# Optimization experiments

Hardware: AMD Instinct MI355X
Metric: run time of the kernel (lower is better)

Reference implementation:

```python
import jax, jax.numpy as jnp
import numpy as np

M, N, E, IN, C, HID, TOPK = 4, 50000, 400000, 128, 128, 256, 2
NEG_SLOPE = 0.2


def setup_inputs() -> dict:
    key = jax.random.key(0)
    k = jax.random.split(key, 16)
    s = lambda f: 1.0 / np.sqrt(f)
    return {
        "x_src": jax.random.normal(k[0], (M, N, IN), jnp.float32),
        "x_dst": jax.random.normal(k[1], (N, IN), jnp.float32),
        "src_idx": jax.random.randint(k[2], (M, E), 0, N),
        "dst_idx": jax.random.randint(k[3], (M, E), 0, N),
        "proj_Ws": jax.random.normal(k[4], (M, IN, C), jnp.float32) * s(IN),
        "proj_bs": jnp.zeros((M, C), jnp.float32),
        "projd_W": jax.random.normal(k[5], (IN, C), jnp.float32) * s(IN),
        "projd_b": jnp.zeros((C,), jnp.float32),
        "lin_src": jax.random.normal(k[6], (M, C), jnp.float32) * s(C),
        "lin_dst": jax.random.normal(k[7], (M, C), jnp.float32) * s(C),
        "gm_W1": jax.random.normal(k[8], (C, C), jnp.float32) * s(C),
        "gm_b1": jnp.zeros((C,), jnp.float32),
        "gm_W2": jax.random.normal(k[9], (C, C), jnp.float32) * s(C),
        "gm_b2": jnp.zeros((C,), jnp.float32),
        "gate_W1": jax.random.normal(k[10], (M * C, HID), jnp.float32) * s(M * C),
        "gate_b1": jnp.zeros((HID,), jnp.float32),
        "gate_W2": jax.random.normal(k[11], (HID, M), jnp.float32) * s(HID),
        "gate_b2": jnp.zeros((M,), jnp.float32),
        "exp_W1": jax.random.normal(k[12], (M, C, HID), jnp.float32) * s(C),
        "exp_b1": jnp.zeros((M, HID), jnp.float32),
        "exp_W2": jax.random.normal(k[13], (M, HID, C), jnp.float32) * s(HID),
        "exp_b2": jnp.zeros((M, C), jnp.float32),
    }


def _propagate(xs_t, asrc_t, adst_t, si, di, recept_t):
    # GAT-style attention message passing for one edge type.
    # xs_t: [N,C] projected src feats, asrc_t/adst_t: [N] attn logits,
    # si/di: [E] edge endpoints, recept_t: [N] per-dst-node receptivity gate.
    e = jax.nn.leaky_relu(asrc_t[si] + adst_t[di], NEG_SLOPE)  # [E]
    emax = jax.ops.segment_max(e, di, num_segments=N)
    ez = jnp.exp(e - emax[di])
    den = jax.ops.segment_sum(ez, di, num_segments=N)
    alpha = ez / (den[di] + 1e-16)                             # softmax per dst node
    msg = xs_t[si] * (alpha * recept_t[di])[:, None]           # [E,C]
    return jax.ops.segment_sum(msg, di, num_segments=N)       # [N,C]


def reference(x_src, x_dst, src_idx, dst_idx, proj_Ws, proj_bs, projd_W, projd_b,
              lin_src, lin_dst, gm_W1, gm_b1, gm_W2, gm_b2,
              gate_W1, gate_b1, gate_W2, gate_b2,
              exp_W1, exp_b1, exp_W2, exp_b2):
    # --- SynapticConvLayer (eval path, heads=1) ---
    xs = jnp.einsum('mni,mic->mnc', x_src, proj_Ws) + proj_bs[:, None, :]  # [M,N,C]
    xd = x_dst @ projd_W + projd_b                                          # [N,C]
    a_src = jnp.einsum('mnc,mc->mn', xs, lin_src)
    a_dst = jnp.einsum('nc,mc->mn', xd[None].repeat(M, 0) * 0 + xd[None], lin_dst) if False else jnp.einsum('nc,mc->mn', xd, lin_dst)
    prop = jax.vmap(_propagate)
    out1 = prop(xs, a_src, a_dst, src_idx, dst_idx, jnp.ones((M, N), xs.dtype))
    # receptivity from grad_map surrogate (inference branch)
    feat_diff = out1 - xd[None]                                            # [M,N,C]
    mo = jax.nn.sigmoid(jax.nn.relu(feat_diff @ gm_W1 + gm_b1) @ gm_W2 + gm_b2)
    gd = (mo * feat_diff).mean(axis=-1)                                    # [M,N]
    recept = gd / (jnp.abs(gd) + 1e-8)                                     # L2-norm over the singleton head dim == abs
    out2 = prop(xs, a_src, a_dst, src_idx, dst_idx, recept)
    feats = jax.nn.relu(out2)                                              # [M,N,C] per-edge-type dst features
    # --- SourceExpertMoE ---
    feats_nm = feats.transpose(1, 0, 2)                                    # [N,M,C]
    gate_in = feats_nm.reshape(N, M * C)
    logits = jax.nn.relu(gate_in @ gate_W1 + gate_b1) @ gate_W2 + gate_b2
    gw = jax.nn.softmax(logits, axis=1)
    scores = gw + recept.T                                                 # gate weights + receptivity
    top_w, top_i = jax.lax.top_k(scores, TOPK)
    top_w = top_w / top_w.sum(axis=1, keepdims=True)
    # expert e applied to source-e features for every node (dense, then gather top-k)
    h = jax.nn.relu(jnp.einsum('nmi,mih->nmh', feats_nm, exp_W1) + exp_b1)
    out_all = jnp.einsum('nmh,mho->nmo', h, exp_W2) + exp_b2               # [N,M,C]
    sel = jnp.take_along_axis(out_all, top_i[:, :, None], axis=1)          # [N,K,C]
    final = (sel * top_w[:, :, None]).sum(axis=1)                          # [N,C]
    return final
```

## Files before the change

### kernel.cpp

```cpp
#include <hip/hip_runtime.h>
#include <hip/hip_bf16.h>
#include <math.h>

#define M_  4
#define N_  50000
#define E_  400000
#define IN_ 128
#define C_  128
#define HID_ 256

template<int AMODE, int EPI, int ASCALE>
__global__ void __launch_bounds__(256) gemm8(
    const float* A, const float* A2, const float* __restrict__ B,
    const float* __restrict__ bias, float* Cmat,
    const float* __restrict__ rowscale, const int* __restrict__ idx,
    const int* __restrict__ cnts, const float* __restrict__ AS,
    const float* __restrict__ fdbuf, const int* __restrict__ roff,
    int R, int K, int NC,
    long long aBatch, long long bBatch, int biasBatch, long long cBatch,
    long long strideM)
{
  __shared__ float As[8][128];
  __shared__ float Bs[8][128];
  __shared__ float red[(EPI == 5) ? 128 * 17 : 1];

  const int tid = threadIdx.x;
  const int b = blockIdx.y;
  const int Reff = (AMODE == 4 || AMODE == 5) ? cnts[b] : (cnts ? cnts[0] : R);
  const int rb = blockIdx.x * 128;
  if (rb >= Reff) return;
  const int cb = blockIdx.z * 128;

  const float* Ab = (AMODE == 2) ? A : (A + (long long)b * aBatch);
  const float* Bb = B + (long long)b * bBatch + cb;
  const float* biasb = bias + (long long)b * biasBatch + cb;

  const int ar = tid >> 1;
  const int ak = (tid & 1) * 4;
  const int r_a = rb + ar;
  const bool a_ok = (r_a < Reff);
  long long a_row = 0;
  float a_rs = 0.f;
  if (a_ok) {
    if (AMODE == 3) {
      int orow = idx[r_a];
      a_row = (long long)orow * K;
      if (ASCALE == 2) a_rs = AS[orow];
    } else if (AMODE == 4) {
      int orow = idx[(long long)b * N_ + r_a];
      a_row = (long long)orow * K;
      if (ASCALE == 2) a_rs = AS[(long long)b * N_ + orow];
    } else if (AMODE == 5) {
      a_row = (long long)(roff[b] + r_a) * K;
    } else if (AMODE == 2) {
      a_row = (long long)r_a * 128;
    } else {
      a_row = (long long)r_a * K;
    }
  }
  const int bk = tid >> 5;
  const int bc = (tid & 31) * 4;

  const int tx = tid & 15;
  const int ty = tid >> 4;

  float acc[8][8];
  #pragma unroll
  for (int i = 0; i < 8; ++i)
    #pragma unroll
    for (int j = 0; j < 8; ++j) acc[i][j] = 0.f;

  const int nt = K >> 3;
  float4 av = make_float4(0.f, 0.f, 0.f, 0.f), bv;

  if (a_ok) {
    if (AMODE == 2) {
      av = *(const float4*)(Ab + (long long)(ak >> 7) * strideM + a_row + (ak & 127));
      if (ASCALE == 1) {
        float rs = AS[(ak >> 7) * N_ + r_a];
        av.x = fmaxf(av.x * rs, 0.f); av.y = fmaxf(av.y * rs, 0.f);
        av.z = fmaxf(av.z * rs, 0.f); av.w = fmaxf(av.w * rs, 0.f);
      }
    } else {
      av = *(const float4*)(Ab + a_row + ak);
      if (AMODE == 1) {
        float4 y = *(const float4*)(A2 + (long long)r_a * 128 + ak);
        av.x -= y.x; av.y -= y.y; av.z -= y.z; av.w -= y.w;
      }
      if ((AMODE == 3 || AMODE == 4) && ASCALE == 2) {
        av.x = fmaxf(av.x * a_rs, 0.f); av.y = fmaxf(av.y * a_rs, 0.f);
        av.z = fmaxf(av.z * a_rs, 0.f); av.w = fmaxf(av.w * a_rs, 0.f);
      }
    }
  }
  bv = *(const float4*)(Bb + (long long)bk * NC + bc);

  for (int t = 0; t < nt; ++t) {
    __syncthreads();
    As[ak + 0][ar] = av.x; As[ak + 1][ar] = av.y;
    As[ak + 2][ar] = av.z; As[ak + 3][ar] = av.w;
    *(float4*)(&Bs[bk][bc]) = bv;
    __syncthreads();

    if (t + 1 < nt) {
      const int k0 = (t + 1) * 8;
      if (a_ok) {
        if (AMODE == 2) {
          int kk0 = k0 + ak;
          av = *(const float4*)(Ab + (long long)(kk0 >> 7) * strideM + a_row + (kk0 & 127));
          if (ASCALE == 1) {
            float rs = AS[(kk0 >> 7) * N_ + r_a];
            av.x = fmaxf(av.x * rs, 0.f); av.y = fmaxf(av.y * rs, 0.f);
            av.z = fmaxf(av.z * rs, 0.f); av.w = fmaxf(av.w * rs, 0.f);
          }
        } else {
          av = *(const float4*)(Ab + a_row + k0 + ak);
          if (AMODE == 1) {
            float4 y = *(const float4*)(A2 + (long long)r_a * 128 + k0 + ak);
            av.x -= y.x; av.y -= y.y; av.z -= y.z; av.w -= y.w;
          }
          if ((AMODE == 3 || AMODE == 4) && ASCALE == 2) {
            av.x = fmaxf(av.x * a_rs, 0.f); av.y = fmaxf(av.y * a_rs, 0.f);
            av.z = fmaxf(av.z * a_rs, 0.f); av.w = fmaxf(av.w * a_rs, 0.f);
          }
        }
      }
      bv = *(const float4*)(Bb + (long long)(k0 + bk) * NC + bc);
    }

    #pragma unroll
    for (int kk = 0; kk < 8; ++kk) {
      float4 alo = *(float4*)(&As[kk][ty * 4]);
      float4 ahi = *(float4*)(&As[kk][64 + ty * 4]);
      float4 blo = *(float4*)(&Bs[kk][tx * 4]);
      float4 bhi = *(float4*)(&Bs[kk][64 + tx * 4]);
      float a8[8] = {alo.x, alo.y, alo.z, alo.w, ahi.x, ahi.y, ahi.z, ahi.w};
      float b8[8] = {blo.x, blo.y, blo.z, blo.w, bhi.x, bhi.y, bhi.z, bhi.w};
      #pragma unroll
      for (int i = 0; i < 8; ++i)
        #pragma unroll
        for (int j = 0; j < 8; ++j)
          acc[i][j] += a8[i] * b8[j];
    }
  }

  if (EPI == 5) {
    #pragma unroll
    for (int i = 0; i < 8; ++i) {
      const int r_local = (i < 4 ? ty * 4 + i : 64 + ty * 4 + (i - 4));
      const int r = rb + r_local;
      if (r < Reff) {
        const float* fdrow = fdbuf + (long long)b * cBatch + (long long)r * 128;
        const float* xdrow = A2 + (long long)r * 128;
        float4 flo = *(const float4*)(fdrow + tx * 4);
        float4 fhi = *(const float4*)(fdrow + 64 + tx * 4);
        float4 xlo = *(const float4*)(xdrow + tx * 4);
        float4 xhi = *(const float4*)(xdrow + 64 + tx * 4);
        float fd8[8] = {flo.x - xlo.x, flo.y - xlo.y, flo.z - xlo.z, flo.w - xlo.w,
                        fhi.x - xhi.x, fhi.y - xhi.y, fhi.z - xhi.z, fhi.w - xhi.w};
        float p = 0.f;
        #pragma unroll
        for (int j = 0; j < 8; ++j) {
          const int c = (j < 4 ? tx * 4 + j : 64 + tx * 4 + (j - 4));
          float mo = 1.f / (1.f + expf(-(acc[i][j] + biasb[c])));
          p += mo * fd8[j];
        }
        red[r_local * 17 + tx] = p;
      }
    }
    __syncthreads();
    if (tid < 128) {
      const int r = rb + tid;
      if (r < Reff) {
        float s = 0.f;
        #pragma unroll
        for (int t = 0; t < 16; ++t) s += red[tid * 17 + t];
        float gd = s / 128.f;
        Cmat[(long long)b * N_ + r] = gd / (fabsf(gd) + 1e-8f);
      }
    }
    return;
  }

  #pragma unroll
  for (int i = 0; i < 8; ++i) {
    const int r = rb + (i < 4 ? ty * 4 + i : 64 + ty * 4 + (i - 4));
    if (r >= Reff) continue;
    long long crow;
    float w = 0.f;
    if (EPI == 4) {
      int orow = idx[r];
      w = rowscale[orow];
      crow = (long long)orow * NC + cb;
    } else if (EPI == 8) {
      int orow = idx[(long long)b * N_ + r];
      w = rowscale[(long long)b * N_ + orow];
      crow = (long long)orow * 128 + cb;
    } else if (EPI == 7) {
      crow = (long long)(roff[b] + r) * NC + cb;
    } else {
      crow = (long long)b * cBatch + (long long)r * NC + cb;
    }
    #pragma unroll
    for (int j = 0; j < 8; ++j) {
      const int c = (j < 4 ? tx * 4 + j : 64 + tx * 4 + (j - 4));
      float v = acc[i][j] + biasb[c];
      if (EPI == 1 || EPI == 7) v = fmaxf(v, 0.f);
      if (EPI == 2) v = 1.f / (1.f + expf(-v));
      if (EPI == 4) Cmat[crow + c] += w * v;
      else if (EPI == 8) atomicAdd(&Cmat[crow + c], w * v);
      else Cmat[crow + c] = v;
    }
  }
}

__global__ void attn_logit_kernel(const float* __restrict__ X, const float* __restrict__ lin,
                                  float* __restrict__ out, int Nn, int perM)
{
  int m = blockIdx.y;
  int w = blockIdx.x * (blockDim.x >> 6) + (threadIdx.x >> 6);
  int lane = threadIdx.x & 63;
  if (w >= Nn) return;
  long long row = perM ? ((long long)m * Nn + w) : (long long)w;
  const float* xr = X + row * 128;
  const float* lr = lin + m * 128;
  float acc = xr[lane] * lr[lane] + xr[lane + 64] * lr[lane + 64];
  #pragma unroll
  for (int off = 32; off > 0; off >>= 1) acc += __shfl_down(acc, off);
  if (lane == 0) out[(long long)m * Nn + w] = acc;
}

__global__ void count_kernel(const int* __restrict__ dst, int* __restrict__ cnt, int Nn)
{
  int e = blockIdx.x * blockDim.x + threadIdx.x;
  int m = blockIdx.y;
  if (e >= E_) return;
  atomicAdd(&cnt[(long long)m * Nn + dst[(long long)m * E_ + e]], 1);
}

__global__ void chunkscan_kernel(const int* __restrict__ cnt, int* __restrict__ rowptr,
                                 int* __restrict__ chunktot)
{
  int m = blockIdx.y, ch = blockIdx.x;
  int base = ch * 1024;
  const int* c = cnt + (long long)m * N_;
  int* rp = rowptr + (long long)m * (N_ + 1);
  __shared__ int sums[256];
  int t = threadIdx.x;
  int v[4]; int s = 0;
  #pragma unroll
  for (int k = 0; k < 4; ++k) {
    int i = base + t * 4 + k;
    v[k] = (i < N_) ? c[i] : 0;
    s += v[k];
  }
  sums[t] = s;
  __syncthreads();
  for (int off = 1; off < 256; off <<= 1) {
    int x = (t >= off) ? sums[t - off] : 0;
    __syncthreads();
    sums[t] += x;
    __syncthreads();
  }
  int run = sums[t] - s;
  #pragma unroll
  for (int k = 0; k < 4; ++k) {
    int i = base + t * 4 + k;
    run += v[k];
    if (i < N_) rp[i + 1] = run;
  }
  if (t == 255) chunktot[m * 64 + ch] = sums[255];
}

__global__ void scantot_kernel(int* __restrict__ chunktot, int nch)
{
  int m = threadIdx.x;
  if (m >= M_) return;
  int run = 0;
  for (int ch = 0; ch < nch; ++ch) {
    int v = chunktot[m * 64 + ch];
    chunktot[m * 64 + ch] = run;
    run += v;
  }
}

__global__ void addoff_kernel(int* __restrict__ rowptr, const int* __restrict__ chunktot)
{
  int m = blockIdx.y, ch = blockIdx.x;
  int off = chunktot[m * 64 + ch];
  int t = threadIdx.x;
  int* rp = rowptr + (long long)m * (N_ + 1);
  #pragma unroll
  for (int k = 0; k < 4; ++k) {
    int i = ch * 1024 + t * 4 + k;
    if (i < N_) rp[i + 1] += off;
  }
  if (ch == 0 && t == 0) rp[0] = 0;
}

__global__ void scatter_kernel(const int* __restrict__ dst, const int* __restrict__ rowptr,
                               int* __restrict__ fill, int* __restrict__ col, int Nn)
{
  int e = blockIdx.x * blockDim.x + threadIdx.x;
  int m = blockIdx.y;
  if (e >= E_) return;
  int d = dst[(long long)m * E_ + e];
  int pos = rowptr[(long long)m * (Nn + 1) + d] + atomicAdd(&fill[(long long)m * Nn + d], 1);
  col[(long long)m * E_ + pos] = e;
}

__global__ void sortbucket_kernel(const int* __restrict__ rowptr, int* __restrict__ col, int Nn)
{
  int n = blockIdx.x * blockDim.x + threadIdx.x;
  int m = blockIdx.y;
  if (n >= Nn) return;
  const int* rp = rowptr + (long long)m * (Nn + 1);
  int* c = col + (long long)m * E_;
  int b = rp[n], e = rp[n + 1];
  for (int i = b + 1; i < e; ++i) {
    int v = c[i]; int j = i - 1;
    while (j >= b && c[j] > v) { c[j + 1] = c[j]; --j; }
    c[j + 1] = v;
  }
}

__global__ void edge_e_kernel(const int* __restrict__ src, const int* __restrict__ dst,
                              const float* __restrict__ asrc, const float* __restrict__ adst,
                              float* __restrict__ e_edge)
{
  int e = blockIdx.x * blockDim.x + threadIdx.x;
  int m = blockIdx.y;
  if (e >= E_) return;
  long long off = (long long)m * E_ + e;
  float v = asrc[(long long)m * N_ + src[off]] + adst[(long long)m * N_ + dst[off]];
  e_edge[off] = (v >= 0.f) ? v : 0.2f * v;
}

__global__ void alpha_kernel(const int* __restrict__ rowptr, const int* __restrict__ col,
                             const int* __restrict__ src, const float* __restrict__ e_edge,
                             float* __restrict__ alpha, int* __restrict__ src_csr)
{
  int n = blockIdx.x * blockDim.x + threadIdx.x;
  int m = blockIdx.y;
  if (n >= N_) return;
  const int* rp = rowptr + (long long)m * (N_ + 1);
  const int* cl = col + (long long)m * E_;
  const int* sr = src + (long long)m * E_;
  const float* ee = e_edge + (long long)m * E_;
  float* al = alpha + (long long)m * E_;
  int* sc = src_csr + (long long)m * E_;
  int b = rp[n], en = rp[n + 1];
  if (b == en) return;
  float emax = -INFINITY;
  for (int j = b; j < en; ++j) emax = fmaxf(emax, ee[cl[j]]);
  float den = 0.f;
  for (int j = b; j < en; ++j) {
    int eid = cl[j];
    float ez = expf(ee[eid] - emax);
    den += ez;
    al[j] = ez;
    sc[j] = sr[eid];
  }
  float inv = 1.f / (den + 1e-16f);
  for (int j = b; j < en; ++j) al[j] *= inv;
}

__global__ void prop2_kernel(const float* __restrict__ xs, const int* __restrict__ rowptr,
                             const float* __restrict__ alpha, const int* __restrict__ src_csr,
                             float* __restrict__ out)
{
  int d = blockIdx.x * 2 + (threadIdx.x >> 7);
  int m = blockIdx.y;
  int c = threadIdx.x & 127;
  if (d >= N_) return;
  const int* rp = rowptr + (long long)m * (N_ + 1);
  const float* al = alpha + (long long)m * E_;
  const int* sc = src_csr + (long long)m * E_;
  const float* xsm = xs + (long long)m * N_ * 128;
  int b = rp[d], en = rp[d + 1];
  float acc = 0.f;
  int j = b;
  for (; j + 3 < en; j += 4) {
    float a0 = al[j], a1 = al[j + 1], a2 = al[j + 2], a3 = al[j + 3];
    int s0 = sc[j], s1 = sc[j + 1], s2 = sc[j + 2], s3 = sc[j + 3];
    float x0 = xsm[(long long)s0 * 128 + c];
    float x1 = xsm[(long long)s1 * 128 + c];
    float x2 = xsm[(long long)s2 * 128 + c];
    float x3 = xsm[(long long)s3 * 128 + c];
    acc += a0 * x0; acc += a1 * x1; acc += a2 * x2; acc += a3 * x3;
  }
  for (; j < en; ++j)
    acc += al[j] * xsm[(long long)sc[j] * 128 + c];
  out[((long long)m * N_ + d) * 128 + c] = acc;
}

__global__ void gate_logits_kernel(const float* __restrict__ h, const float* __restrict__ W2,
                                   const float* __restrict__ b2, float* __restrict__ logits, int Nn)
{
  int w = blockIdx.x * (blockDim.x >> 6) + (threadIdx.x >> 6);
  int lane = threadIdx.x & 63;
  if (w >= Nn) return;
  const float* hr = h + (long long)w * 256;
  float a0 = 0.f, a1 = 0.f, a2 = 0.f, a3 = 0.f;
  for (int j = lane; j < 256; j += 64) {
    float hv = hr[j];
    a0 += hv * W2[j * 4 + 0];
    a1 += hv * W2[j * 4 + 1];
    a2 += hv * W2[j * 4 + 2];
    a3 += hv * W2[j * 4 + 3];
  }
  #pragma unroll
  for (int off = 32; off > 0; off >>= 1) {
    a0 += __shfl_down(a0, off);
    a1 += __shfl_down(a1, off);
    a2 += __shfl_down(a2, off);
    a3 += __shfl_down(a3, off);
  }
  if (lane == 0) {
    long long o = (long long)w * 4;
    logits[o + 0] = a0 + b2[0];
    logits[o + 1] = a1 + b2[1];
    logits[o + 2] = a2 + b2[2];
    logits[o + 3] = a3 + b2[3];
  }
}

__global__ void topk_kernel(const float* __restrict__ logits, const float* __restrict__ recept,
                            float* __restrict__ wsel, int Nn)
{
  int n = blockIdx.x * blockDim.x + threadIdx.x;
  if (n >= Nn) return;
  float l[4];
  #pragma unroll
  for (int m = 0; m < 4; ++m) l[m] = logits[(long long)n * 4 + m];
  float mx = fmaxf(fmaxf(l[0], l[1]), fmaxf(l[2], l[3]));
  float e[4], s = 0.f;
  #pragma unroll
  for (int m = 0; m < 4; ++m) { e[m] = expf(l[m] - mx); s += e[m]; }
  float sc[4];
  #pragma unroll
  for (int m = 0; m < 4; ++m) sc[m] = e[m] / s + recept[(long long)m * Nn + n];
  int i0 = 0; float v0 = sc[0];
  #pragma unroll
  for (int m = 1; m < 4; ++m) if (sc[m] > v0) { v0 = sc[m]; i0 = m; }
  int i1 = -1; float v1 = -INFINITY;
  #pragma unroll
  for (int m = 0; m < 4; ++m) { if (m == i0) continue; if (sc[m] > v1) { v1 = sc[m]; i1 = m; } }
  float ts = v0 + v1;
  float w0 = v0 / ts, w1 = v1 / ts;
  #pragma unroll
  for (int m = 0; m < 4; ++m)
    wsel[(long long)m * Nn + n] = (m == i0) ? w0 : ((m == i1) ? w1 : 0.f);
}

__global__ void compact_kernel(const float* __restrict__ wsel, int* __restrict__ idx,
                               int* __restrict__ cnts, int Nn)
{
  int n = blockIdx.x * blockDim.x + threadIdx.x;
  if (n >= Nn) return;
  #pragma unroll
  for (int m = 0; m < 4; ++m) {
    if (wsel[(long long)m * Nn + n] != 0.f) {
      int p = atomicAdd(&cnts[m], 1);
      idx[(long long)m * Nn + p] = n;
    }
  }
}

__global__ void prefix4_kernel(const int* __restrict__ cnts, int* __restrict__ off)
{
  if (threadIdx.x == 0) {
    int r = 0;
    #pragma unroll
    for (int m = 0; m < 4; ++m) { off[m] = r; r += cnts[m]; }
  }
}

extern "C" void kernel_launch(void* const* d_in, const int* in_sizes, int n_in,
                              void* d_out, int out_size, void* d_ws, size_t ws_size,
                              hipStream_t stream) {
  const float* x_src   = (const float*)d_in[0];
  const float* x_dst   = (const float*)d_in[1];
  const int*   src_idx = (const int*)d_in[2];
  const int*   dst_idx = (const int*)d_in[3];
  const float* proj_Ws = (const float*)d_in[4];
  const float* proj_bs = (const float*)d_in[5];
  const float* projd_W = (const float*)d_in[6];
  const float* projd_b = (const float*)d_in[7];
  const float* lin_src = (const float*)d_in[8];
  const float* lin_dst = (const float*)d_in[9];
  const float* gm_W1   = (const float*)d_in[10];
  const float* gm_b1   = (const float*)d_in[11];
  const float* gm_W2   = (const float*)d_in[12];
  const float* gm_b2   = (const float*)d_in[13];
  const float* gate_W1 = (const float*)d_in[14];
  const float* gate_b1 = (const float*)d_in[15];
  const float* gate_W2 = (const float*)d_in[16];
  const float* gate_b2 = (const float*)d_in[17];
  const float* exp_W1  = (const float*)d_in[18];
  const float* exp_b1  = (const float*)d_in[19];
  const float* exp_W2  = (const float*)d_in[20];
  const float* exp_b2  = (const float*)d_in[21];
  float* final_out = (float*)d_out;

  float* ws = (float*)d_ws;
  float* bufA   = ws;
  float* bufB   = ws + 25600000LL;
  float* xd     = ws + 51200000LL;
  float* asrc   = ws + 57600000LL;
  float* adst   = ws + 57800000LL;
  float* recept = ws + 58000000LL;
  float* wsel   = ws + 58200000LL;
  float* logits = ws + 58400000LL;
  float* e_edge = ws + 58600000LL;
  float* alpha  = ws + 60200000LL;
  int*   ibase  = (int*)(ws + 61800000LL);
  int*   rowptr = ibase;
  int*   col    = ibase + 200004;
  int*   cnt    = ibase + 1800004;
  int*   expidx = cnt;
  int*   expcnt = ibase + 2000004;
  int*   src_csr= ibase + 2000008;
  int*   chunktot = ibase + 3600008;
  int*   expoff = ibase + 3600264;

  const long long NC = (long long)N_ * C_;
  const int RB = (N_ + 127) / 128;
  const int NCH = (N_ + 1023) / 1024;

  hipMemsetAsync(d_out, 0, (size_t)out_size * sizeof(float), stream);

  hipMemsetAsync(cnt, 0, (size_t)M_ * N_ * sizeof(int), stream);
  count_kernel<<<dim3((E_ + 255) / 256, M_), 256, 0, stream>>>(dst_idx, cnt, N_);
  chunkscan_kernel<<<dim3(NCH, M_), 256, 0, stream>>>(cnt, rowptr, chunktot);
  scantot_kernel<<<1, 64, 0, stream>>>(chunktot, NCH);
  addoff_kernel<<<dim3(NCH, M_), 256, 0, stream>>>(rowptr, chunktot);
  hipMemsetAsync(cnt, 0, (size_t)M_ * N_ * sizeof(int), stream);
  scatter_kernel<<<dim3((E_ + 255) / 256, M_), 256, 0, stream>>>(dst_idx, rowptr, cnt, col, N_);
  sortbucket_kernel<<<dim3((N_ + 255) / 256, M_), 256, 0, stream>>>(rowptr, col, N_);

  gemm8<0, 0, 0><<<dim3(RB, 1, 1), 256, 0, stream>>>(
      x_dst, nullptr, projd_W, projd_b, xd, nullptr, nullptr, nullptr, nullptr, nullptr,
      nullptr, N_, IN_, C_, 0, 0, 0, 0, 0);
  attn_logit_kernel<<<dim3((N_ + 3) / 4, M_), 256, 0, stream>>>(xd, lin_dst, adst, N_, 0);

  gemm8<0, 0, 0><<<dim3(RB, M_, 1), 256, 0, stream>>>(
      x_src, nullptr, proj_Ws, proj_bs, bufA, nullptr, nullptr, nullptr, nullptr, nullptr,
      nullptr, N_, IN_, C_, NC, (long long)IN_ * C_, C_, NC, 0);
  attn_logit_kernel<<<dim3((N_ + 3) / 4, M_), 256, 0, stream>>>(bufA, lin_src, asrc, N_, 1);

  edge_e_kernel<<<dim3((E_ + 255) / 256, M_), 256, 0, stream>>>(
      src_idx, dst_idx, asrc, adst, e_edge);
  alpha_kernel<<<dim3((N_ + 255) / 256, M_), 256, 0, stream>>>(
      rowptr, col, src_idx, e_edge, alpha, src_csr);

  prop2_kernel<<<dim3((N_ + 1) / 2, M_), 256, 0, stream>>>(bufA, rowptr, alpha, src_csr, bufB);

  gemm8<1, 1, 0><<<dim3(RB, M_, 1), 256, 0, stream>>>(
      bufB, xd, gm_W1, gm_b1, bufA, nullptr, nullptr, nullptr, nullptr, nullptr,
      nullptr, N_, C_, C_, NC, 0, 0, NC, 0);
  gemm8<0, 5, 0><<<dim3(RB, M_, 1), 256, 0, stream>>>(
      bufA, xd, gm_W2, gm_b2, recept, nullptr, nullptr, nullptr, nullptr, bufB,
      nullptr, N_, C_, C_, NC, 0, 0, NC, 0);

  gemm8<2, 1, 1><<<dim3(RB, 1, 2), 256, 0, stream>>>(
      bufB, nullptr, gate_W1, gate_b1, bufA, nullptr, nullptr, nullptr, recept, nullptr,
      nullptr, N_, M_ * C_, HID_, 0, 0, 0, 0, NC);
  gate_logits_kernel<<<dim3((N_ + 3) / 4), 256, 0, stream>>>(bufA, gate_W2, gate_b2, logits, N_);
  topk_kernel<<<(N_ + 255) / 256, 256, 0, stream>>>(logits, recept, wsel, N_);

  hipMemsetAsync(expcnt, 0, 4 * sizeof(int), stream);
  compact_kernel<<<(N_ + 255) / 256, 256, 0, stream>>>(wsel, expidx, expcnt, N_);
  prefix4_kernel<<<1, 64, 0, stream>>>(expcnt, expoff);

  gemm8<4, 7, 2><<<dim3(RB, M_, 2), 256, 0, stream>>>(
      bufB, nullptr, exp_W1, exp_b1, bufA, nullptr,
      expidx, expcnt, recept, nullptr, expoff,
      N_, C_, HID_, NC, (long long)C_ * HID_, HID_, 0, 0);
  gemm8<5, 8, 0><<<dim3(RB, M_, 1), 256, 0, stream>>>(
      bufA, nullptr, exp_W2, exp_b2, final_out, wsel,
      expidx, expcnt, nullptr, nullptr, expoff,
      N_, HID_, C_, 0, (long long)HID_ * C_, C_, 0, 0);
}
```

Before: 1.379 ms.

## Double-buffer GEMM shared tiles and replace atomic expert scatter with combine kernel

The GEMM now ping-pongs two shared-memory tile buffers, so each k-step needs one barrier instead of two and the next tile's global loads overlap the current FMAs. The expert second-layer GEMM writes dense per-expert outputs into a compact buffer instead of atomically adding weighted rows into the output. A new combine kernel then gathers each node's selected expert rows via a recorded position map and sums them with the gate weights. This drops the output memset and the atomics, but adds an extra kernel pass and doubles the shared memory for the tiles.

```diff
diff --git a/kernel.cpp b/kernel.cpp
--- a/kernel.cpp
+++ b/kernel.cpp
@@ -10,18 +10,18 @@
 #define HID_ 256
 
 template<int AMODE, int EPI, int ASCALE>
-__global__ void __launch_bounds__(256) gemm8(
+__global__ void __launch_bounds__(256) gemm9(
     const float* A, const float* A2, const float* __restrict__ B,
     const float* __restrict__ bias, float* Cmat,
-    const float* __restrict__ rowscale, const int* __restrict__ idx,
-    const int* __restrict__ cnts, const float* __restrict__ AS,
-    const float* __restrict__ fdbuf, const int* __restrict__ roff,
+    const int* __restrict__ idx, const int* __restrict__ cnts,
+    const float* __restrict__ AS, const float* __restrict__ fdbuf,
+    const int* __restrict__ roff,
     int R, int K, int NC,
     long long aBatch, long long bBatch, int biasBatch, long long cBatch,
     long long strideM)
 {
-  __shared__ float As[8][128];
-  __shared__ float Bs[8][128];
+  __shared__ float As[2][8][128];
+  __shared__ float Bs[2][8][128];
   __shared__ float red[(EPI == 5) ? 128 * 17 : 1];
 
   const int tid = threadIdx.x;
@@ -42,11 +42,7 @@
   long long a_row = 0;
   float a_rs = 0.f;
   if (a_ok) {
-    if (AMODE == 3) {
-      int orow = idx[r_a];
-      a_row = (long long)orow * K;
-      if (ASCALE == 2) a_rs = AS[orow];
-    } else if (AMODE == 4) {
+    if (AMODE == 4) {
       int orow = idx[(long long)b * N_ + r_a];
       a_row = (long long)orow * K;
       if (ASCALE == 2) a_rs = AS[(long long)b * N_ + orow];
@@ -73,67 +69,57 @@
   const int nt = K >> 3;
   float4 av = make_float4(0.f, 0.f, 0.f, 0.f), bv;
 
-  if (a_ok) {
-    if (AMODE == 2) {
-      av = *(const float4*)(Ab + (long long)(ak >> 7) * strideM + a_row + (ak & 127));
-      if (ASCALE == 1) {
-        float rs = AS[(ak >> 7) * N_ + r_a];
-        av.x = fmaxf(av.x * rs, 0.f); av.y = fmaxf(av.y * rs, 0.f);
-        av.z = fmaxf(av.z * rs, 0.f); av.w = fmaxf(av.w * rs, 0.f);
-      }
-    } else {
-      av = *(const float4*)(Ab + a_row + ak);
-      if (AMODE == 1) {
-        float4 y = *(const float4*)(A2 + (long long)r_a * 128 + ak);
-        av.x -= y.x; av.y -= y.y; av.z -= y.z; av.w -= y.w;
-      }
-      if ((AMODE == 3 || AMODE == 4) && ASCALE == 2) {
-        av.x = fmaxf(av.x * a_rs, 0.f); av.y = fmaxf(av.y * a_rs, 0.f);
-        av.z = fmaxf(av.z * a_rs, 0.f); av.w = fmaxf(av.w * a_rs, 0.f);
-      }
-    }
-  }
-  bv = *(const float4*)(Bb + (long long)bk * NC + bc);
+#define LOAD_TILE(k0)                                                          \
+  {                                                                            \
+    if (a_ok) {                                                                \
+      if (AMODE == 2) {                                                        \
+        int kk0 = (k0) + ak;                                                   \
+        av = *(const float4*)(Ab + (long long)(kk0 >> 7) * strideM + a_row +   \
+                              (kk0 & 127));                                    \
+        if (ASCALE == 1) {                                                     \
+          float rs = AS[(kk0 >> 7) * N_ + r_a];                                \
+          av.x = fmaxf(av.x * rs, 0.f); av.y = fmaxf(av.y * rs, 0.f);          \
+          av.z = fmaxf(av.z * rs, 0.f); av.w = fmaxf(av.w * rs, 0.f);          \
+        }                                                                      \
+      } else {                                                                 \
+        av = *(const float4*)(Ab + a_row + (k0) + ak);                         \
+        if (AMODE == 1) {                                                      \
+          float4 y = *(const float4*)(A2 + (long long)r_a * 128 + (k0) + ak);  \
+          av.x -= y.x; av.y -= y.y; av.z -= y.z; av.w -= y.w;                  \
+        }                                                                      \
+        if (AMODE == 4 && ASCALE == 2) {                                       \
+          av.x = fmaxf(av.x * a_rs, 0.f); av.y = fmaxf(av.y * a_rs, 0.f);      \
+          av.z = fmaxf(av.z * a_rs, 0.f); av.w = fmaxf(av.w * a_rs, 0.f);      \
+        }                                                                      \
+      }                                                                        \
+    } else {                                                                   \
+      av = make_float4(0.f, 0.f, 0.f, 0.f);                                    \
+    }                                                                          \
+    bv = *(const float4*)(Bb + (long long)((k0) + bk) * NC + bc);              \
+  }
+
+#define WRITE_TILE(buf)                                                        \
+  {                                                                            \
+    As[buf][ak + 0][ar] = av.x; As[buf][ak + 1][ar] = av.y;                    \
+    As[buf][ak + 2][ar] = av.z; As[buf][ak + 3][ar] = av.w;                    \
+    *(float4*)(&Bs[buf][bk][bc]) = bv;                                         \
+  }
+
+  LOAD_TILE(0)
+  WRITE_TILE(0)
 
   for (int t = 0; t < nt; ++t) {
     __syncthreads();
-    As[ak + 0][ar] = av.x; As[ak + 1][ar] = av.y;
-    As[ak + 2][ar] = av.z; As[ak + 3][ar] = av.w;
-    *(float4*)(&Bs[bk][bc]) = bv;
-    __syncthreads();
-
-    if (t + 1 < nt) {
-      const int k0 = (t + 1) * 8;
-      if (a_ok) {
-        if (AMODE == 2) {
-          int kk0 = k0 + ak;
-          av = *(const float4*)(Ab + (long long)(kk0 >> 7) * strideM + a_row + (kk0 & 127));
-          if (ASCALE == 1) {
-            float rs = AS[(kk0 >> 7) * N_ + r_a];
-            av.x = fmaxf(av.x * rs, 0.f); av.y = fmaxf(av.y * rs, 0.f);
-            av.z = fmaxf(av.z * rs, 0.f); av.w = fmaxf(av.w * rs, 0.f);
-          }
-        } else {
-          av = *(const float4*)(Ab + a_row + k0 + ak);
-          if (AMODE == 1) {
-            float4 y = *(const float4*)(A2 + (long long)r_a * 128 + k0 + ak);
-            av.x -= y.x; av.y -= y.y; av.z -= y.z; av.w -= y.w;
-          }
-          if ((AMODE == 3 || AMODE == 4) && ASCALE == 2) {
-            av.x = fmaxf(av.x * a_rs, 0.f); av.y = fmaxf(av.y * a_rs, 0.f);
-            av.z = fmaxf(av.z * a_rs, 0.f); av.w = fmaxf(av.w * a_rs, 0.f);
-          }
-        }
-      }
-      bv = *(const float4*)(Bb + (long long)(k0 + bk) * NC + bc);
-    }
+    const int cur = t & 1;
+    const bool more = (t + 1 < nt);
+    if (more) LOAD_TILE((t + 1) * 8)
 
     #pragma unroll
     for (int kk = 0; kk < 8; ++kk) {
-      float4 alo = *(float4*)(&As[kk][ty * 4]);
-      float4 ahi = *(float4*)(&As[kk][64 + ty * 4]);
-      float4 blo = *(float4*)(&Bs[kk][tx * 4]);
-      float4 bhi = *(float4*)(&Bs[kk][64 + tx * 4]);
+      float4 alo = *(float4*)(&As[cur][kk][ty * 4]);
+      float4 ahi = *(float4*)(&As[cur][kk][64 + ty * 4]);
+      float4 blo = *(float4*)(&Bs[cur][kk][tx * 4]);
+      float4 bhi = *(float4*)(&Bs[cur][kk][64 + tx * 4]);
       float a8[8] = {alo.x, alo.y, alo.z, alo.w, ahi.x, ahi.y, ahi.z, ahi.w};
       float b8[8] = {blo.x, blo.y, blo.z, blo.w, bhi.x, bhi.y, bhi.z, bhi.w};
       #pragma unroll
@@ -142,7 +128,11 @@
         for (int j = 0; j < 8; ++j)
           acc[i][j] += a8[i] * b8[j];
     }
-  }
+
+    if (more) WRITE_TILE(cur ^ 1)
+  }
+#undef LOAD_TILE
+#undef WRITE_TILE
 
   if (EPI == 5) {
     #pragma unroll
@@ -187,29 +177,15 @@
     const int r = rb + (i < 4 ? ty * 4 + i : 64 + ty * 4 + (i - 4));
     if (r >= Reff) continue;
     long long crow;
-    float w = 0.f;
-    if (EPI == 4) {
-      int orow = idx[r];
-      w = rowscale[orow];
-      crow = (long long)orow * NC + cb;
-    } else if (EPI == 8) {
-      int orow = idx[(long long)b * N_ + r];
-      w = rowscale[(long long)b * N_ + orow];
-      crow = (long long)orow * 128 + cb;
-    } else if (EPI == 7) {
-      crow = (long long)(roff[b] + r) * NC + cb;
-    } else {
-      crow = (long long)b * cBatch + (long long)r * NC + cb;
-    }
+    if (EPI == 7) crow = (long long)(roff[b] + r) * NC + cb;
+    else if (EPI == 9) crow = (long long)(roff[b] + r) * 128 + cb;
+    else crow = (long long)b * cBatch + (long long)r * NC + cb;
     #pragma unroll
     for (int j = 0; j < 8; ++j) {
       const int c = (j < 4 ? tx * 4 + j : 64 + tx * 4 + (j - 4));
       float v = acc[i][j] + biasb[c];
       if (EPI == 1 || EPI == 7) v = fmaxf(v, 0.f);
-      if (EPI == 2) v = 1.f / (1.f + expf(-v));
-      if (EPI == 4) Cmat[crow + c] += w * v;
-      else if (EPI == 8) atomicAdd(&Cmat[crow + c], w * v);
-      else Cmat[crow + c] = v;
+      Cmat[crow + c] = v;
     }
   }
 }
@@ -454,7 +430,7 @@
 }
 
 __global__ void compact_kernel(const float* __restrict__ wsel, int* __restrict__ idx,
-                               int* __restrict__ cnts, int Nn)
+                               int* __restrict__ posmn, int* __restrict__ cnts, int Nn)
 {
   int n = blockIdx.x * blockDim.x + threadIdx.x;
   if (n >= Nn) return;
@@ -463,6 +439,7 @@
     if (wsel[(long long)m * Nn + n] != 0.f) {
       int p = atomicAdd(&cnts[m], 1);
       idx[(long long)m * Nn + p] = n;
+      posmn[(long long)m * Nn + n] = p;
     }
   }
 }
@@ -474,6 +451,27 @@
     #pragma unroll
     for (int m = 0; m < 4; ++m) { off[m] = r; r += cnts[m]; }
   }
+}
+
+__global__ void combine_kernel(const float* __restrict__ outp, const float* __restrict__ wsel,
+                               const int* __restrict__ posmn, const int* __restrict__ expoff,
+                               float* __restrict__ fin)
+{
+  long long i = (long long)blockIdx.x * blockDim.x + threadIdx.x;
+  if (i >= (long long)N_ * 32) return;
+  int n = (int)(i >> 5);
+  int c4 = (int)(i & 31) * 4;
+  float4 acc = make_float4(0.f, 0.f, 0.f, 0.f);
+  #pragma unroll
+  for (int m = 0; m < 4; ++m) {
+    float w = wsel[(long long)m * N_ + n];
+    if (w != 0.f) {
+      int p = expoff[m] + posmn[(long long)m * N_ + n];
+      float4 v = *(const float4*)(outp + (long long)p * 128 + c4);
+      acc.x += w * v.x; acc.y += w * v.y; acc.z += w * v.z; acc.w += w * v.w;
+    }
+  }
+  *(float4*)(fin + (long long)n * 128 + c4) = acc;
 }
 
 extern "C" void kernel_launch(void* const* d_in, const int* in_sizes, int n_in,
@@ -523,12 +521,11 @@
   int*   src_csr= ibase + 2000008;
   int*   chunktot = ibase + 3600008;
   int*   expoff = ibase + 3600264;
+  int*   posmn  = ibase + 3600268;
 
   const long long NC = (long long)N_ * C_;
   const int RB = (N_ + 127) / 128;
   const int NCH = (N_ + 1023) / 1024;
-
-  hipMemsetAsync(d_out, 0, (size_t)out_size * sizeof(float), stream);
 
   hipMemsetAsync(cnt, 0, (size_t)M_ * N_ * sizeof(int), stream);
   count_kernel<<<dim3((E_ + 255) / 256, M_), 256, 0, stream>>>(dst_idx, cnt, N_);
@@ -539,13 +536,13 @@
   scatter_kernel<<<dim3((E_ + 255) / 256, M_), 256, 0, stream>>>(dst_idx, rowptr, cnt, col, N_);
   sortbucket_kernel<<<dim3((N_ + 255) / 256, M_), 256, 0, stream>>>(rowptr, col, N_);
 
-  gemm8<0, 0, 0><<<dim3(RB, 1, 1), 256, 0, stream>>>(
-      x_dst, nullptr, projd_W, projd_b, xd, nullptr, nullptr, nullptr, nullptr, nullptr,
+  gemm9<0, 0, 0><<<dim3(RB, 1, 1), 256, 0, stream>>>(
+      x_dst, nullptr, projd_W, projd_b, xd, nullptr, nullptr, nullptr, nullptr,
       nullptr, N_, IN_, C_, 0, 0, 0, 0, 0);
   attn_logit_kernel<<<dim3((N_ + 3) / 4, M_), 256, 0, stream>>>(xd, lin_dst, adst, N_, 0);
 
-  gemm8<0, 0, 0><<<dim3(RB, M_, 1), 256, 0, stream>>>(
-      x_src, nullptr, proj_Ws, proj_bs, bufA, nullptr, nullptr, nullptr, nullptr, nullptr,
+  gemm9<0, 0, 0><<<dim3(RB, M_, 1), 256, 0, stream>>>(
+      x_src, nullptr, proj_Ws, proj_bs, bufA, nullptr, nullptr, nullptr, nullptr,
       nullptr, N_, IN_, C_, NC, (long long)IN_ * C_, C_, NC, 0);
   attn_logit_kernel<<<dim3((N_ + 3) / 4, M_), 256, 0, stream>>>(bufA, lin_src, asrc, N_, 1);
 
@@ -556,29 +553,29 @@
 
   prop2_kernel<<<dim3((N_ + 1) / 2, M_), 256, 0, stream>>>(bufA, rowptr, alpha, src_csr, bufB);
 
-  gemm8<1, 1, 0><<<dim3(RB, M_, 1), 256, 0, stream>>>(
-      bufB, xd, gm_W1, gm_b1, bufA, nullptr, nullptr, nullptr, nullptr, nullptr,
+  gemm9<1, 1, 0><<<dim3(RB, M_, 1), 256, 0, stream>>>(
+      bufB, xd, gm_W1, gm_b1, bufA, nullptr, nullptr, nullptr, nullptr,
       nullptr, N_, C_, C_, NC, 0, 0, NC, 0);
-  gemm8<0, 5, 0><<<dim3(RB, M_, 1), 256, 0, stream>>>(
-      bufA, xd, gm_W2, gm_b2, recept, nullptr, nullptr, nullptr, nullptr, bufB,
+  gemm9<0, 5, 0><<<dim3(RB, M_, 1), 256, 0, stream>>>(
+      bufA, xd, gm_W2, gm_b2, recept, nullptr, nullptr, nullptr, bufB,
       nullptr, N_, C_, C_, NC, 0, 0, NC, 0);
 
-  gemm8<2, 1, 1><<<dim3(RB, 1, 2), 256, 0, stream>>>(
-      bufB, nullptr, gate_W1, gate_b1, bufA, nullptr, nullptr, nullptr, recept, nullptr,
+  gemm9<2, 1, 1><<<dim3(RB, 1, 2), 256, 0, stream>>>(
+      bufB, nullptr, gate_W1, gate_b1, bufA, nullptr, nullptr, recept, nullptr,
       nullptr, N_, M_ * C_, HID_, 0, 0, 0, 0, NC);
   gate_logits_kernel<<<dim3((N_ + 3) / 4), 256, 0, stream>>>(bufA, gate_W2, gate_b2, logits, N_);
   topk_kernel<<<(N_ + 255) / 256, 256, 0, stream>>>(logits, recept, wsel, N_);
 
   hipMemsetAsync(expcnt, 0, 4 * sizeof(int), stream);
-  compact_kernel<<<(N_ + 255) / 256, 256, 0, stream>>>(wsel, expidx, expcnt, N_);
+  compact_kernel<<<(N_ + 255) / 256, 256, 0, stream>>>(wsel, expidx, posmn, expcnt, N_);
   prefix4_kernel<<<1, 64, 0, stream>>>(expcnt, expoff);
 
-  gemm8<4, 7, 2><<<dim3(RB, M_, 2), 256, 0, stream>>>(
-      bufB, nullptr, exp_W1, exp_b1, bufA, nullptr,
-      expidx, expcnt, recept, nullptr, expoff,
-      N_, C_, HID_, NC, (long long)C_ * HID_, HID_, 0, 0);
-  gemm8<5, 8, 0><<<dim3(RB, M_, 1), 256, 0, stream>>>(
-      bufA, nullptr, exp_W2, exp_b2, final_out, wsel,
-      expidx, expcnt, nullptr, nullptr, expoff,
-      N_, HID_, C_, 0, (long long)HID_ * C_, C_, 0, 0);
-}
+  gemm9<4, 7, 2><<<dim3(RB, M_, 2), 256, 0, stream>>>(
+      bufB, nullptr, exp_W1, exp_b1, bufA, expidx, expcnt, recept, nullptr,
+      expoff, N_, C_, HID_, NC, (long long)C_ * HID_, HID_, 0, 0);
+  gemm9<5, 9, 0><<<dim3(RB, M_, 1), 256, 0, stream>>>(
+      bufA, nullptr, exp_W2, exp_b2, bufB, expidx, expcnt, nullptr, nullptr,
+      expoff, N_, HID_, C_, 0, (long long)HID_ * C_, C_, 0, 0);
+  combine_kernel<<<(int)(((long long)N_ * 32 + 255) / 256), 256, 0, stream>>>(
+      bufB, wsel, posmn, expoff, final_out);
+}
```

After: 1.348 ms. 2.2% less time.
